# Optimization experiments

Measured on AMD Instinct MI355X. Metric: run time of the kernel, lower is better.

## Reference

```python
import jax, jax.numpy as jnp
import numpy as np

FIELD_DIMS = [26000] * 39
EMBED_DIM = 64
MLP_DIMS = [400, 400, 400]
BATCH = 16384
OFFSETS = jnp.asarray(np.concatenate(([0], np.cumsum(FIELD_DIMS)[:-1])), dtype=jnp.int32)
BN_INV = 1.0 / np.sqrt(1.0 + 1e-5)  # eval-mode BatchNorm1d: running_mean=0, running_var=1


def setup_inputs() -> dict:
    key = jax.random.key(0)
    ks = jax.random.split(key, 16)
    B, F, E = BATCH, len(FIELD_DIMS), EMBED_DIM
    V = sum(FIELD_DIMS)
    s = lambda k, shp, sc=0.05: (jax.random.normal(k, shp, jnp.float32) * sc)
    inp = {
        "x": jax.random.randint(ks[0], (B, F), 0, FIELD_DIMS[0], dtype=jnp.int32),
        "emb_table": s(ks[1], (V, E)),
        "lin_table": s(ks[2], (V, 1)),
        "lin_bias": jnp.zeros((1,), jnp.float32),
        "sparse_var": s(ks[3], (F, E), 0.1),
        "Wt": s(ks[4], (F, E, E)),  # per-field Linear weights, (out,in) layout
        "bt": jnp.zeros((F, E), jnp.float32),
    }
    dims = [F * E] + MLP_DIMS
    for i in range(3):
        inp[f"W{i+1}"] = s(ks[5 + i], (dims[i], dims[i + 1]))
        inp[f"b{i+1}"] = jnp.zeros((dims[i + 1],), jnp.float32)
        inp[f"g{i+1}"] = jnp.ones((dims[i + 1],), jnp.float32)
        inp[f"be{i+1}"] = jnp.zeros((dims[i + 1],), jnp.float32)
    inp["Wout"] = s(ks[9], (MLP_DIMS[-1], 1))
    inp["bout"] = jnp.zeros((1,), jnp.float32)
    return inp


def reference(x, emb_table, lin_table, lin_bias, sparse_var, Wt, bt,
              W1, b1, g1, be1, W2, b2, g2, be2, W3, b3, g3, be3, Wout, bout):
    B = x.shape[0]
    idx = x + OFFSETS[None, :]                       # (B, F) global vocab ids
    # sparse gate (detached in torch), eval-mode hard threshold mask
    sv = jax.nn.sigmoid(jax.lax.stop_gradient(sparse_var) * 15.0)
    sv = jnp.where(sv > 0.001, sv, 0.0)              # (F, E)
    embed_x = emb_table[idx] * sv                    # (B, F, E) gather + gate
    # per-field small Linear, batched as one einsum (torch: y = e @ W.T + b)
    trans = jnp.einsum('bfi,foi->bfo', embed_x, Wt) + bt  # (B, F, E)
    # FM second-order term
    sum_f = trans.sum(axis=1)                        # (B, E)
    fm = 0.5 * jnp.sum(sum_f * sum_f - (trans * trans).sum(axis=1),
                       axis=-1, keepdims=True)       # (B, 1)
    # first-order linear term
    lin = lin_table[idx].sum(axis=1) + lin_bias      # (B, 1)
    # MLP on flattened gated embeddings (Linear -> BN(eval) -> ReLU)
    h = embed_x.reshape(B, -1)
    for W, b, g, be in ((W1, b1, g1, be1), (W2, b2, g2, be2), (W3, b3, g3, be3)):
        h = jax.nn.relu((h @ W + b) * (BN_INV * g) + be)
    mlp = h @ Wout + bout                            # (B, 1)
    return jax.nn.sigmoid(jnp.squeeze(lin + fm + mlp, axis=1))  # (B,)
```

## Files before the change

kernel.cpp:

```cpp
#include <hip/hip_runtime.h>

#define BT 16384
#define NF 39
#define FD 26000

typedef unsigned short u16;
typedef unsigned int u32;
typedef short bf16x8 __attribute__((ext_vector_type(8)));
typedef float f32x4 __attribute__((ext_vector_type(4)));

__device__ __forceinline__ float bf2f(u16 h) {
  union { u32 u; float f; } v; v.u = ((u32)h) << 16; return v.f;
}
__device__ __forceinline__ u16 f2bf(float f) {
  union { float f; u32 u; } v; v.f = f;
  u32 r = v.u + 0x7fffu + ((v.u >> 16) & 1u);
  return (u16)(r >> 16);
}

__device__ __forceinline__ void gld16(const u16* g, u16* l) {
  __builtin_amdgcn_global_load_lds(
      (const __attribute__((address_space(1))) void*)g,
      (__attribute__((address_space(3))) void*)l, 16, 0, 0);
}

__global__ __launch_bounds__(256) void k_embed(
    const int* __restrict__ x, const float* __restrict__ emb,
    const float* __restrict__ lin_table, const float* __restrict__ lin_bias,
    const float* __restrict__ sparse_var, const float* __restrict__ Wt,
    const float* __restrict__ bt, u16* __restrict__ h0, float* __restrict__ base)
{
  __shared__ u16                s_x[32 * NF];
  __shared__ float              s_sv[NF * 64];
  __shared__ float              s_bt[NF * 64];
  __shared__ __align__(16) u16  s_emb[32 * 72];
  __shared__ __align__(16) u16  s_wt[64 * 72];
  __shared__ float              s_S[32 * 65];
  __shared__ float              s_Qp[64];
  __shared__ float              s_lin[32];

  const int tid = threadIdx.x;
  const int b0 = blockIdx.x * 32;

  for (int i = tid; i < 32 * NF; i += 256) s_x[i] = (u16)x[b0 * NF + i];
  for (int i = tid; i < NF * 64; i += 256) {
    float v = sparse_var[i];
    float s = 1.0f / (1.0f + __expf(-15.0f * v));
    s_sv[i] = (s > 0.001f) ? s : 0.0f;
    s_bt[i] = bt[i];
  }
  __syncthreads();

  const int wave = tid >> 6, lane = tid & 63;
  const int quad = lane >> 4, c16 = lane & 15;
  const int mt = wave & 1, nh = wave >> 1;

  float q[4] = {0.f, 0.f, 0.f, 0.f};
  float accS[2][4];
  #pragma unroll
  for (int j = 0; j < 2; ++j)
    #pragma unroll
    for (int r = 0; r < 4; ++r) accS[j][r] = 0.f;

  const int g_row = tid >> 3, g_c8 = (tid & 7) * 8;

  for (int f = 0; f < NF; ++f) {
    #pragma unroll
    for (int it = 0; it < 2; ++it) {
      int row = g_row + it * 32;
      float4 w0 = *(const float4*)&Wt[f * 4096 + row * 64 + g_c8];
      float4 w1 = *(const float4*)&Wt[f * 4096 + row * 64 + g_c8 + 4];
      union { uint4 v; u16 h[8]; } p;
      p.h[0] = f2bf(w0.x); p.h[1] = f2bf(w0.y); p.h[2] = f2bf(w0.z); p.h[3] = f2bf(w0.w);
      p.h[4] = f2bf(w1.x); p.h[5] = f2bf(w1.y); p.h[6] = f2bf(w1.z); p.h[7] = f2bf(w1.w);
      *(uint4*)&s_wt[row * 72 + g_c8] = p.v;
    }
    {
      long gi = (long)((int)s_x[g_row * NF + f] + f * FD);
      float4 e0 = *(const float4*)&emb[gi * 64 + g_c8];
      float4 e1 = *(const float4*)&emb[gi * 64 + g_c8 + 4];
      union { uint4 v; u16 h[8]; } p;
      p.h[0] = f2bf(e0.x * s_sv[f * 64 + g_c8 + 0]);
      p.h[1] = f2bf(e0.y * s_sv[f * 64 + g_c8 + 1]);
      p.h[2] = f2bf(e0.z * s_sv[f * 64 + g_c8 + 2]);
      p.h[3] = f2bf(e0.w * s_sv[f * 64 + g_c8 + 3]);
      p.h[4] = f2bf(e1.x * s_sv[f * 64 + g_c8 + 4]);
      p.h[5] = f2bf(e1.y * s_sv[f * 64 + g_c8 + 5]);
      p.h[6] = f2bf(e1.z * s_sv[f * 64 + g_c8 + 6]);
      p.h[7] = f2bf(e1.w * s_sv[f * 64 + g_c8 + 7]);
      *(uint4*)&s_emb[g_row * 72 + g_c8] = p.v;
      *(uint4*)&h0[(long)(b0 + g_row) * 2496 + f * 64 + g_c8] = p.v;
    }
    __syncthreads();

    bf16x8 a0 = *(const bf16x8*)&s_emb[(mt * 16 + c16) * 72 + quad * 8];
    bf16x8 a1 = *(const bf16x8*)&s_emb[(mt * 16 + c16) * 72 + 32 + quad * 8];
    #pragma unroll
    for (int j = 0; j < 2; ++j) {
      int nt = nh * 2 + j;
      bf16x8 bb0 = *(const bf16x8*)&s_wt[(nt * 16 + c16) * 72 + quad * 8];
      bf16x8 bb1 = *(const bf16x8*)&s_wt[(nt * 16 + c16) * 72 + 32 + quad * 8];
      f32x4 acc = {0.f, 0.f, 0.f, 0.f};
      acc = __builtin_amdgcn_mfma_f32_16x16x32_bf16(a0, bb0, acc, 0, 0, 0);
      acc = __builtin_amdgcn_mfma_f32_16x16x32_bf16(a1, bb1, acc, 0, 0, 0);
      float btv = s_bt[f * 64 + nt * 16 + c16];
      #pragma unroll
      for (int r = 0; r < 4; ++r) {
        float t = acc[r] + btv;
        accS[j][r] += t;
        q[r] += t * t;
      }
    }
    __syncthreads();
  }

  #pragma unroll
  for (int j = 0; j < 2; ++j)
    #pragma unroll
    for (int r = 0; r < 4; ++r)
      s_S[(mt * 16 + quad * 4 + r) * 65 + (nh * 2 + j) * 16 + c16] = accS[j][r];

  #pragma unroll
  for (int r = 0; r < 4; ++r) {
    float v = q[r];
    v += __shfl_xor(v, 1, 64);
    v += __shfl_xor(v, 2, 64);
    v += __shfl_xor(v, 4, 64);
    v += __shfl_xor(v, 8, 64);
    if (c16 == 0) s_Qp[nh * 32 + mt * 16 + quad * 4 + r] = v;
  }

  {
    int row = tid >> 3, fi = tid & 7;
    float lv = 0.f;
    for (int f = fi; f < NF; f += 8)
      lv += lin_table[(int)s_x[row * NF + f] + f * FD];
    lv += __shfl_xor(lv, 1, 64);
    lv += __shfl_xor(lv, 2, 64);
    lv += __shfl_xor(lv, 4, 64);
    if (fi == 0) s_lin[row] = lv;
  }
  __syncthreads();

  if (tid < 32) {
    float s2 = 0.f;
    #pragma unroll 8
    for (int e = 0; e < 64; ++e) { float v = s_S[tid * 65 + e]; s2 += v * v; }
    float fmv = 0.5f * (s2 - (s_Qp[tid] + s_Qp[32 + tid]));
    base[b0 + tid] = s_lin[tid] + lin_bias[0] + fmv;
  }
}

__global__ __launch_bounds__(256) void k_gemm(
    const u16* __restrict__ A, int lda, const u16* __restrict__ Bt, int ldb,
    int kit, const float* __restrict__ bias, const float* __restrict__ g,
    const float* __restrict__ be, u16* __restrict__ C, int ldc)
{
  __shared__ __align__(16) u16 sA[128 * 64];
  __shared__ __align__(16) u16 sB[80 * 64];

  const int tid = threadIdx.x;
  int bid = blockIdx.x;
  int xcd = bid & 7;
  int j = bid >> 3;
  const int m0 = (xcd * 16 + j / 5) * 128;
  const int n0 = (j % 5) * 80;

  const int wave = tid >> 6, lane = tid & 63;
  const int quad = lane >> 4, c16 = lane & 15;

  const int srow = lane >> 3;
  const int sclog = (lane & 7) ^ (srow & 7);
  const u16* gA = A + (long)m0 * lda + sclog * 8;
  const u16* gB = Bt + (long)n0 * ldb + sclog * 8;

  f32x4 acc[2][5];
  #pragma unroll
  for (int mtt = 0; mtt < 2; ++mtt)
    #pragma unroll
    for (int nt = 0; nt < 5; ++nt) acc[mtt][nt] = {0.f, 0.f, 0.f, 0.f};

  for (int kk = 0; kk < kit; ++kk) {
    const int k0 = kk * 64;
    #pragma unroll
    for (int it = 0; it < 4; ++it) {
      int s = wave * 4 + it;
      gld16(gA + (long)(s * 8 + srow) * lda + k0, &sA[s * 512]);
    }
    gld16(gB + (long)(wave * 8 + srow) * ldb + k0, &sB[wave * 512]);
    gld16(gB + (long)((wave + 4) * 8 + srow) * ldb + k0, &sB[(wave + 4) * 512]);
    if (wave < 2)
      gld16(gB + (long)((wave + 8) * 8 + srow) * ldb + k0, &sB[(wave + 8) * 512]);
    __syncthreads();

    #pragma unroll
    for (int ks = 0; ks < 2; ++ks) {
      const int co = ((ks * 4 + quad) ^ (c16 & 7)) * 8;
      bf16x8 a0 = *(const bf16x8*)&sA[(wave * 32 + c16) * 64 + co];
      bf16x8 a1 = *(const bf16x8*)&sA[(wave * 32 + 16 + c16) * 64 + co];
      #pragma unroll
      for (int nt = 0; nt < 5; ++nt) {
        bf16x8 b = *(const bf16x8*)&sB[(nt * 16 + c16) * 64 + co];
        acc[0][nt] = __builtin_amdgcn_mfma_f32_16x16x32_bf16(a0, b, acc[0][nt], 0, 0, 0);
        acc[1][nt] = __builtin_amdgcn_mfma_f32_16x16x32_bf16(a1, b, acc[1][nt], 0, 0, 0);
      }
    }
    __syncthreads();
  }

  const float BN_INV = 0.9999950000374997f;
  #pragma unroll
  for (int nt = 0; nt < 5; ++nt) {
    int col = n0 + nt * 16 + c16;
    float bb = bias[col];
    float sc = BN_INV * g[col];
    float bv = be[col];
    #pragma unroll
    for (int mtt = 0; mtt < 2; ++mtt) {
      #pragma unroll
      for (int r = 0; r < 4; ++r) {
        int row = m0 + wave * 32 + mtt * 16 + quad * 4 + r;
        float y = (acc[mtt][nt][r] + bb) * sc + bv;
        y = fmaxf(y, 0.f);
        C[(long)row * ldc + col] = f2bf(y);
      }
    }
  }
  if (ldc > 400 && n0 == 320) {
    int npad = ldc - 400;
    for (int s = tid; s < 128 * npad; s += 256) {
      int rr = s / npad, cc = s % npad;
      C[(long)(m0 + rr) * ldc + 400 + cc] = 0;
    }
  }
}

__global__ __launch_bounds__(256) void k_transpose3(
    const float* __restrict__ W1, u16* __restrict__ W1T,
    const float* __restrict__ W2, u16* __restrict__ W2T,
    const float* __restrict__ W3, u16* __restrict__ W3T)
{
  int z = blockIdx.z;
  const float* in = (z == 0) ? W1 : (z == 1) ? W2 : W3;
  u16* out = (z == 0) ? W1T : (z == 1) ? W2T : W3T;
  int R = (z == 0) ? 2496 : 400;
  int Rpad = (z == 0) ? 2496 : 448;
  const int C = 400;
  int r0 = blockIdx.y * 32, c0 = blockIdx.x * 32;
  if (r0 >= Rpad) return;
  __shared__ u16 t[32][33];
  int tx = threadIdx.x & 31, ty = threadIdx.x >> 5;
  for (int i = ty; i < 32; i += 8) {
    int r = r0 + i, c = c0 + tx;
    t[i][tx] = (r < R && c < C) ? f2bf(in[(long)r * C + c]) : (u16)0;
  }
  __syncthreads();
  for (int i = ty; i < 32; i += 8) {
    int c = c0 + i, r = r0 + tx;
    if (c < C && r < Rpad) out[(long)c * Rpad + r] = t[tx][i];
  }
}

__global__ __launch_bounds__(256) void k_final(
    const u16* __restrict__ h3, const float* __restrict__ Wout,
    const float* __restrict__ bout, const float* __restrict__ base,
    float* __restrict__ out)
{
  int wave = threadIdx.x >> 6, lane = threadIdx.x & 63;
  int b = blockIdx.x * 4 + wave;
  float s = 0.f;
  for (int jj = lane; jj < 400; jj += 64)
    s += bf2f(h3[(long)b * 448 + jj]) * Wout[jj];
  #pragma unroll
  for (int m = 32; m >= 1; m >>= 1) s += __shfl_xor(s, m, 64);
  if (lane == 0) {
    float z = s + base[b] + bout[0];
    out[b] = 1.0f / (1.0f + __expf(-z));
  }
}

extern "C" void kernel_launch(void* const* d_in, const int* in_sizes, int n_in,
                              void* d_out, int out_size, void* d_ws, size_t ws_size,
                              hipStream_t stream)
{
  const int*   x         = (const int*)d_in[0];
  const float* emb       = (const float*)d_in[1];
  const float* lin_table = (const float*)d_in[2];
  const float* lin_bias  = (const float*)d_in[3];
  const float* svar      = (const float*)d_in[4];
  const float* Wt        = (const float*)d_in[5];
  const float* bt        = (const float*)d_in[6];
  const float* W1  = (const float*)d_in[7];
  const float* b1  = (const float*)d_in[8];
  const float* g1  = (const float*)d_in[9];
  const float* be1 = (const float*)d_in[10];
  const float* W2  = (const float*)d_in[11];
  const float* b2  = (const float*)d_in[12];
  const float* g2  = (const float*)d_in[13];
  const float* be2 = (const float*)d_in[14];
  const float* W3  = (const float*)d_in[15];
  const float* b3  = (const float*)d_in[16];
  const float* g3  = (const float*)d_in[17];
  const float* be3 = (const float*)d_in[18];
  const float* Wo  = (const float*)d_in[19];
  const float* bo  = (const float*)d_in[20];

  char* ws = (char*)d_ws;
  size_t off = 0;
  u16* h0 = (u16*)(ws + off);   off += (size_t)BT * 2496 * 2;
  u16* h1 = (u16*)(ws + off);   off += (size_t)BT * 448 * 2;
  u16* h2 = (u16*)(ws + off);   off += (size_t)BT * 448 * 2;
  u16* h3 = (u16*)(ws + off);   off += (size_t)BT * 448 * 2;
  float* base = (float*)(ws + off); off += (size_t)BT * 4;
  u16* W1T = (u16*)(ws + off);  off += (size_t)400 * 2496 * 2;
  u16* W2T = (u16*)(ws + off);  off += (size_t)400 * 448 * 2;
  u16* W3T = (u16*)(ws + off);  off += (size_t)400 * 448 * 2;
  (void)ws_size; (void)in_sizes; (void)n_in; (void)out_size;

  k_transpose3<<<dim3(13, 78, 3), 256, 0, stream>>>(W1, W1T, W2, W2T, W3, W3T);
  k_embed<<<512, 256, 0, stream>>>(x, emb, lin_table, lin_bias, svar, Wt, bt,
                                   h0, base);
  k_gemm<<<640, 256, 0, stream>>>(h0, 2496, W1T, 2496, 39, b1, g1, be1, h1, 448);
  k_gemm<<<640, 256, 0, stream>>>(h1, 448, W2T, 448, 7, b2, g2, be2, h2, 448);
  k_gemm<<<640, 256, 0, stream>>>(h2, 448, W3T, 448, 7, b3, g3, be3, h3, 448);
  k_final<<<4096, 256, 0, stream>>>(h3, Wo, bo, base, (float*)d_out);
}
```

Baseline: 480.0 us.

## Fuse embedding with first MLP layer and fuse remaining layers into one tail kernel

The embedding/FM kernel now also computes the first MLP GEMM directly from the gated embeddings held in shared memory, so the large h0 activation is no longer written to or read from global memory. Layers two and three plus the output dot product and sigmoid are merged into a single per-32-row kernel that keeps activations in swizzled LDS. The per-field Wt matrices are converted to bf16 once in a prep kernel, and the weight transposes are padded to 448 columns. The trade-off is that each block handles only 32 rows, so W1 (about 2 MB) is re-streamed by all 512 blocks. Each wave also holds 14 accumulator tiles, which raises register pressure and may reduce occupancy.

```diff
diff --git a/kernel.cpp b/kernel.cpp
--- a/kernel.cpp
+++ b/kernel.cpp
@@ -17,26 +17,75 @@
   u32 r = v.u + 0x7fffu + ((v.u >> 16) & 1u);
   return (u16)(r >> 16);
 }
-
 __device__ __forceinline__ void gld16(const u16* g, u16* l) {
   __builtin_amdgcn_global_load_lds(
       (const __attribute__((address_space(1))) void*)g,
       (__attribute__((address_space(3))) void*)l, 16, 0, 0);
 }
-
-__global__ __launch_bounds__(256) void k_embed(
+__device__ __forceinline__ int swz4(int n) { return (n ^ (n >> 2)) & 3; }
+
+__device__ __forceinline__ void stage_w448(const u16* WT, long ld, int k0,
+                                           u16* s_w, int wave, int lane) {
+  int rlo = lane >> 2, clo = lane & 3;
+  #pragma unroll
+  for (int i = wave; i < 28; i += 4) {
+    int n = i * 16 + rlo;
+    int c = clo ^ swz4(n);
+    gld16(WT + (long)n * ld + k0 + c * 8, &s_w[i * 512]);
+  }
+}
+__device__ __forceinline__ bf16x8 read_b448(const u16* s_w, int n, int quad) {
+  int c = quad ^ swz4(n);
+  return *(const bf16x8*)&s_w[n * 32 + c * 8];
+}
+
+__global__ __launch_bounds__(256) void k_prep(
+    const float* __restrict__ W1, u16* __restrict__ W1T,
+    const float* __restrict__ W2, u16* __restrict__ W2T,
+    const float* __restrict__ W3, u16* __restrict__ W3T,
+    const float* __restrict__ Wt, u16* __restrict__ Wtb)
+{
+  int z = blockIdx.z;
+  if (z == 3) {
+    int idx = (blockIdx.y * 14 + blockIdx.x) * 256 + threadIdx.x;
+    if (idx < NF * 4096) Wtb[idx] = f2bf(Wt[idx]);
+    return;
+  }
+  const float* in = (z == 0) ? W1 : (z == 1) ? W2 : W3;
+  u16* outp = (z == 0) ? W1T : (z == 1) ? W2T : W3T;
+  int K = (z == 0) ? 2496 : 400;
+  int Kpad = (z == 0) ? 2496 : 448;
+  int r0 = blockIdx.y * 32, c0 = blockIdx.x * 32;
+  if (r0 >= Kpad) return;
+  __shared__ u16 t[32][33];
+  int tx = threadIdx.x & 31, ty = threadIdx.x >> 5;
+  for (int i = ty; i < 32; i += 8) {
+    int r = r0 + i, c = c0 + tx;
+    t[i][tx] = (r < K && c < 400) ? f2bf(in[(long)r * 400 + c]) : (u16)0;
+  }
+  __syncthreads();
+  int r = r0 + tx;
+  if (r < Kpad)
+    for (int i = ty; i < 32; i += 8)
+      outp[(long)(c0 + i) * Kpad + r] = t[tx][i];
+}
+
+__global__ __launch_bounds__(256) void k_fused1(
     const int* __restrict__ x, const float* __restrict__ emb,
     const float* __restrict__ lin_table, const float* __restrict__ lin_bias,
-    const float* __restrict__ sparse_var, const float* __restrict__ Wt,
-    const float* __restrict__ bt, u16* __restrict__ h0, float* __restrict__ base)
+    const float* __restrict__ sparse_var, const u16* __restrict__ Wtb,
+    const float* __restrict__ bt, const u16* __restrict__ W1T,
+    const float* __restrict__ b1, const float* __restrict__ g1,
+    const float* __restrict__ be1, u16* __restrict__ h1,
+    float* __restrict__ base)
 {
   __shared__ u16                s_x[32 * NF];
   __shared__ float              s_sv[NF * 64];
   __shared__ float              s_bt[NF * 64];
   __shared__ __align__(16) u16  s_emb[32 * 72];
-  __shared__ __align__(16) u16  s_wt[64 * 72];
-  __shared__ float              s_S[32 * 65];
-  __shared__ float              s_Qp[64];
+  __shared__ __align__(16) u16  s_wt[64 * 64];
+  __shared__ __align__(16) u16  s_w[448 * 32];
+  __shared__ float              s_fm[64];
   __shared__ float              s_lin[32];
 
   const int tid = threadIdx.x;
@@ -54,26 +103,20 @@
   const int wave = tid >> 6, lane = tid & 63;
   const int quad = lane >> 4, c16 = lane & 15;
   const int mt = wave & 1, nh = wave >> 1;
-
+  const int g_row = tid >> 3, g_c8 = (tid & 7) * 8;
+
+  f32x4 acc1[14];
+  #pragma unroll
+  for (int nt = 0; nt < 14; ++nt) acc1[nt] = {0.f, 0.f, 0.f, 0.f};
   float q[4] = {0.f, 0.f, 0.f, 0.f};
-  float accS[2][4];
-  #pragma unroll
-  for (int j = 0; j < 2; ++j)
-    #pragma unroll
-    for (int r = 0; r < 4; ++r) accS[j][r] = 0.f;
-
-  const int g_row = tid >> 3, g_c8 = (tid & 7) * 8;
+  float accS[2][4] = {{0.f,0.f,0.f,0.f},{0.f,0.f,0.f,0.f}};
 
   for (int f = 0; f < NF; ++f) {
-    #pragma unroll
-    for (int it = 0; it < 2; ++it) {
-      int row = g_row + it * 32;
-      float4 w0 = *(const float4*)&Wt[f * 4096 + row * 64 + g_c8];
-      float4 w1 = *(const float4*)&Wt[f * 4096 + row * 64 + g_c8 + 4];
-      union { uint4 v; u16 h[8]; } p;
-      p.h[0] = f2bf(w0.x); p.h[1] = f2bf(w0.y); p.h[2] = f2bf(w0.z); p.h[3] = f2bf(w0.w);
-      p.h[4] = f2bf(w1.x); p.h[5] = f2bf(w1.y); p.h[6] = f2bf(w1.z); p.h[7] = f2bf(w1.w);
-      *(uint4*)&s_wt[row * 72 + g_c8] = p.v;
+    stage_w448(W1T, 2496, f * 64, s_w, wave, lane);
+    #pragma unroll
+    for (int i = 0; i < 2; ++i) {
+      int ii = wave * 2 + i;
+      gld16(Wtb + f * 4096 + ii * 512 + lane * 8, &s_wt[ii * 512]);
     }
     {
       long gi = (long)((int)s_x[g_row * NF + f] + f * FD);
@@ -89,17 +132,17 @@
       p.h[6] = f2bf(e1.z * s_sv[f * 64 + g_c8 + 6]);
       p.h[7] = f2bf(e1.w * s_sv[f * 64 + g_c8 + 7]);
       *(uint4*)&s_emb[g_row * 72 + g_c8] = p.v;
-      *(uint4*)&h0[(long)(b0 + g_row) * 2496 + f * 64 + g_c8] = p.v;
     }
     __syncthreads();
 
     bf16x8 a0 = *(const bf16x8*)&s_emb[(mt * 16 + c16) * 72 + quad * 8];
     bf16x8 a1 = *(const bf16x8*)&s_emb[(mt * 16 + c16) * 72 + 32 + quad * 8];
+
     #pragma unroll
     for (int j = 0; j < 2; ++j) {
       int nt = nh * 2 + j;
-      bf16x8 bb0 = *(const bf16x8*)&s_wt[(nt * 16 + c16) * 72 + quad * 8];
-      bf16x8 bb1 = *(const bf16x8*)&s_wt[(nt * 16 + c16) * 72 + 32 + quad * 8];
+      bf16x8 bb0 = *(const bf16x8*)&s_wt[(nt * 16 + c16) * 64 + quad * 8];
+      bf16x8 bb1 = *(const bf16x8*)&s_wt[(nt * 16 + c16) * 64 + 32 + quad * 8];
       f32x4 acc = {0.f, 0.f, 0.f, 0.f};
       acc = __builtin_amdgcn_mfma_f32_16x16x32_bf16(a0, bb0, acc, 0, 0, 0);
       acc = __builtin_amdgcn_mfma_f32_16x16x32_bf16(a1, bb1, acc, 0, 0, 0);
@@ -111,25 +154,33 @@
         q[r] += t * t;
       }
     }
+    #pragma unroll
+    for (int nt = 0; nt < 14; ++nt) {
+      int n = nh * 224 + nt * 16 + c16;
+      acc1[nt] = __builtin_amdgcn_mfma_f32_16x16x32_bf16(
+          a0, read_b448(s_w, n, quad), acc1[nt], 0, 0, 0);
+    }
     __syncthreads();
-  }
-
-  #pragma unroll
-  for (int j = 0; j < 2; ++j)
-    #pragma unroll
-    for (int r = 0; r < 4; ++r)
-      s_S[(mt * 16 + quad * 4 + r) * 65 + (nh * 2 + j) * 16 + c16] = accS[j][r];
+    stage_w448(W1T, 2496, f * 64 + 32, s_w, wave, lane);
+    __syncthreads();
+    #pragma unroll
+    for (int nt = 0; nt < 14; ++nt) {
+      int n = nh * 224 + nt * 16 + c16;
+      acc1[nt] = __builtin_amdgcn_mfma_f32_16x16x32_bf16(
+          a1, read_b448(s_w, n, quad), acc1[nt], 0, 0, 0);
+    }
+    __syncthreads();
+  }
 
   #pragma unroll
   for (int r = 0; r < 4; ++r) {
-    float v = q[r];
+    float v = accS[0][r] * accS[0][r] + accS[1][r] * accS[1][r] - q[r];
     v += __shfl_xor(v, 1, 64);
     v += __shfl_xor(v, 2, 64);
     v += __shfl_xor(v, 4, 64);
     v += __shfl_xor(v, 8, 64);
-    if (c16 == 0) s_Qp[nh * 32 + mt * 16 + quad * 4 + r] = v;
-  }
-
+    if (c16 == 0) s_fm[nh * 32 + mt * 16 + quad * 4 + r] = v;
+  }
   {
     int row = tid >> 3, fi = tid & 7;
     float lv = 0.f;
@@ -141,141 +192,130 @@
     if (fi == 0) s_lin[row] = lv;
   }
   __syncthreads();
-
-  if (tid < 32) {
-    float s2 = 0.f;
-    #pragma unroll 8
-    for (int e = 0; e < 64; ++e) { float v = s_S[tid * 65 + e]; s2 += v * v; }
-    float fmv = 0.5f * (s2 - (s_Qp[tid] + s_Qp[32 + tid]));
-    base[b0 + tid] = s_lin[tid] + lin_bias[0] + fmv;
-  }
-}
-
-__global__ __launch_bounds__(256) void k_gemm(
-    const u16* __restrict__ A, int lda, const u16* __restrict__ Bt, int ldb,
-    int kit, const float* __restrict__ bias, const float* __restrict__ g,
-    const float* __restrict__ be, u16* __restrict__ C, int ldc)
+  if (tid < 32)
+    base[b0 + tid] = s_lin[tid] + lin_bias[0]
+                   + 0.5f * (s_fm[tid] + s_fm[32 + tid]);
+
+  const float BN_INV = 0.9999950000374997f;
+  #pragma unroll
+  for (int nt = 0; nt < 14; ++nt) {
+    int col = nh * 224 + nt * 16 + c16;
+    bool valid = col < 400;
+    float bb = valid ? b1[col] : 0.f;
+    float sc = valid ? BN_INV * g1[col] : 0.f;
+    float bv = valid ? be1[col] : 0.f;
+    #pragma unroll
+    for (int r = 0; r < 4; ++r) {
+      int row = b0 + mt * 16 + quad * 4 + r;
+      float y = valid ? fmaxf((acc1[nt][r] + bb) * sc + bv, 0.f) : 0.f;
+      h1[(long)row * 448 + col] = f2bf(y);
+    }
+  }
+}
+
+__global__ __launch_bounds__(256) void k_tail(
+    const u16* __restrict__ h1, const u16* __restrict__ W2T,
+    const u16* __restrict__ W3T,
+    const float* __restrict__ b2, const float* __restrict__ g2,
+    const float* __restrict__ be2,
+    const float* __restrict__ b3, const float* __restrict__ g3,
+    const float* __restrict__ be3,
+    const float* __restrict__ Wout, const float* __restrict__ bout,
+    const float* __restrict__ base, float* __restrict__ out)
 {
-  __shared__ __align__(16) u16 sA[128 * 64];
-  __shared__ __align__(16) u16 sB[80 * 64];
+  __shared__ __align__(16) u16 s_h[32 * 448];
+  __shared__ __align__(16) u16 s_w[448 * 32];
+  __shared__ float s_wout[448];
+  __shared__ float s_red[64];
 
   const int tid = threadIdx.x;
-  int bid = blockIdx.x;
-  int xcd = bid & 7;
-  int j = bid >> 3;
-  const int m0 = (xcd * 16 + j / 5) * 128;
-  const int n0 = (j % 5) * 80;
+  const int b0 = blockIdx.x * 32;
+  for (int i = tid; i < 448; i += 256) s_wout[i] = (i < 400) ? Wout[i] : 0.f;
+  for (int s = tid; s < 1792; s += 256) {
+    int flat = s * 8;
+    int row = flat / 448;
+    int kc = (flat - row * 448) >> 3;
+    int pc = (kc & 0x38) | ((kc ^ row) & 7);
+    uint4 v = *(const uint4*)&h1[(long)b0 * 448 + flat];
+    *(uint4*)&s_h[row * 448 + pc * 8] = v;
+  }
+  __syncthreads();
 
   const int wave = tid >> 6, lane = tid & 63;
   const int quad = lane >> 4, c16 = lane & 15;
-
-  const int srow = lane >> 3;
-  const int sclog = (lane & 7) ^ (srow & 7);
-  const u16* gA = A + (long)m0 * lda + sclog * 8;
-  const u16* gB = Bt + (long)n0 * ldb + sclog * 8;
-
-  f32x4 acc[2][5];
-  #pragma unroll
-  for (int mtt = 0; mtt < 2; ++mtt)
-    #pragma unroll
-    for (int nt = 0; nt < 5; ++nt) acc[mtt][nt] = {0.f, 0.f, 0.f, 0.f};
-
-  for (int kk = 0; kk < kit; ++kk) {
-    const int k0 = kk * 64;
-    #pragma unroll
-    for (int it = 0; it < 4; ++it) {
-      int s = wave * 4 + it;
-      gld16(gA + (long)(s * 8 + srow) * lda + k0, &sA[s * 512]);
-    }
-    gld16(gB + (long)(wave * 8 + srow) * ldb + k0, &sB[wave * 512]);
-    gld16(gB + (long)((wave + 4) * 8 + srow) * ldb + k0, &sB[(wave + 4) * 512]);
-    if (wave < 2)
-      gld16(gB + (long)((wave + 8) * 8 + srow) * ldb + k0, &sB[(wave + 8) * 512]);
-    __syncthreads();
-
-    #pragma unroll
-    for (int ks = 0; ks < 2; ++ks) {
-      const int co = ((ks * 4 + quad) ^ (c16 & 7)) * 8;
-      bf16x8 a0 = *(const bf16x8*)&sA[(wave * 32 + c16) * 64 + co];
-      bf16x8 a1 = *(const bf16x8*)&sA[(wave * 32 + 16 + c16) * 64 + co];
+  const int mt = wave & 1, nh = wave >> 1;
+  const int m = mt * 16 + c16;
+  const float BN_INV = 0.9999950000374997f;
+
+  f32x4 acc[14];
+  float p[4] = {0.f, 0.f, 0.f, 0.f};
+
+  for (int layer = 0; layer < 2; ++layer) {
+    const u16* WT = layer ? W3T : W2T;
+    #pragma unroll
+    for (int nt = 0; nt < 14; ++nt) acc[nt] = {0.f, 0.f, 0.f, 0.f};
+    for (int ks = 0; ks < 14; ++ks) {
+      stage_w448(WT, 448, ks * 32, s_w, wave, lane);
+      __syncthreads();
+      int kc = ks * 4 + quad;
+      int pc = (kc & 0x38) | ((kc ^ m) & 7);
+      bf16x8 a = *(const bf16x8*)&s_h[m * 448 + pc * 8];
       #pragma unroll
-      for (int nt = 0; nt < 5; ++nt) {
-        bf16x8 b = *(const bf16x8*)&sB[(nt * 16 + c16) * 64 + co];
-        acc[0][nt] = __builtin_amdgcn_mfma_f32_16x16x32_bf16(a0, b, acc[0][nt], 0, 0, 0);
-        acc[1][nt] = __builtin_amdgcn_mfma_f32_16x16x32_bf16(a1, b, acc[1][nt], 0, 0, 0);
+      for (int nt = 0; nt < 14; ++nt) {
+        int n = nh * 224 + nt * 16 + c16;
+        acc[nt] = __builtin_amdgcn_mfma_f32_16x16x32_bf16(
+            a, read_b448(s_w, n, quad), acc[nt], 0, 0, 0);
       }
-    }
-    __syncthreads();
-  }
-
-  const float BN_INV = 0.9999950000374997f;
-  #pragma unroll
-  for (int nt = 0; nt < 5; ++nt) {
-    int col = n0 + nt * 16 + c16;
-    float bb = bias[col];
-    float sc = BN_INV * g[col];
-    float bv = be[col];
-    #pragma unroll
-    for (int mtt = 0; mtt < 2; ++mtt) {
+      __syncthreads();
+    }
+    if (layer == 0) {
       #pragma unroll
-      for (int r = 0; r < 4; ++r) {
-        int row = m0 + wave * 32 + mtt * 16 + quad * 4 + r;
-        float y = (acc[mtt][nt][r] + bb) * sc + bv;
-        y = fmaxf(y, 0.f);
-        C[(long)row * ldc + col] = f2bf(y);
+      for (int nt = 0; nt < 14; ++nt) {
+        int col = nh * 224 + nt * 16 + c16;
+        bool valid = col < 400;
+        float bb = valid ? b2[col] : 0.f;
+        float sc = valid ? BN_INV * g2[col] : 0.f;
+        float bv = valid ? be2[col] : 0.f;
+        int kc = col >> 3;
+        #pragma unroll
+        for (int r = 0; r < 4; ++r) {
+          int row = mt * 16 + quad * 4 + r;
+          float y = valid ? fmaxf((acc[nt][r] + bb) * sc + bv, 0.f) : 0.f;
+          int pc = (kc & 0x38) | ((kc ^ row) & 7);
+          s_h[row * 448 + pc * 8 + (col & 7)] = f2bf(y);
+        }
       }
-    }
-  }
-  if (ldc > 400 && n0 == 320) {
-    int npad = ldc - 400;
-    for (int s = tid; s < 128 * npad; s += 256) {
-      int rr = s / npad, cc = s % npad;
-      C[(long)(m0 + rr) * ldc + 400 + cc] = 0;
-    }
-  }
-}
-
-__global__ __launch_bounds__(256) void k_transpose3(
-    const float* __restrict__ W1, u16* __restrict__ W1T,
-    const float* __restrict__ W2, u16* __restrict__ W2T,
-    const float* __restrict__ W3, u16* __restrict__ W3T)
-{
-  int z = blockIdx.z;
-  const float* in = (z == 0) ? W1 : (z == 1) ? W2 : W3;
-  u16* out = (z == 0) ? W1T : (z == 1) ? W2T : W3T;
-  int R = (z == 0) ? 2496 : 400;
-  int Rpad = (z == 0) ? 2496 : 448;
-  const int C = 400;
-  int r0 = blockIdx.y * 32, c0 = blockIdx.x * 32;
-  if (r0 >= Rpad) return;
-  __shared__ u16 t[32][33];
-  int tx = threadIdx.x & 31, ty = threadIdx.x >> 5;
-  for (int i = ty; i < 32; i += 8) {
-    int r = r0 + i, c = c0 + tx;
-    t[i][tx] = (r < R && c < C) ? f2bf(in[(long)r * C + c]) : (u16)0;
-  }
-  __syncthreads();
-  for (int i = ty; i < 32; i += 8) {
-    int c = c0 + i, r = r0 + tx;
-    if (c < C && r < Rpad) out[(long)c * Rpad + r] = t[tx][i];
-  }
-}
-
-__global__ __launch_bounds__(256) void k_final(
-    const u16* __restrict__ h3, const float* __restrict__ Wout,
-    const float* __restrict__ bout, const float* __restrict__ base,
-    float* __restrict__ out)
-{
-  int wave = threadIdx.x >> 6, lane = threadIdx.x & 63;
-  int b = blockIdx.x * 4 + wave;
-  float s = 0.f;
-  for (int jj = lane; jj < 400; jj += 64)
-    s += bf2f(h3[(long)b * 448 + jj]) * Wout[jj];
-  #pragma unroll
-  for (int m = 32; m >= 1; m >>= 1) s += __shfl_xor(s, m, 64);
-  if (lane == 0) {
-    float z = s + base[b] + bout[0];
-    out[b] = 1.0f / (1.0f + __expf(-z));
+      __syncthreads();
+    } else {
+      #pragma unroll
+      for (int nt = 0; nt < 14; ++nt) {
+        int col = nh * 224 + nt * 16 + c16;
+        bool valid = col < 400;
+        float bb = valid ? b3[col] : 0.f;
+        float sc = valid ? BN_INV * g3[col] : 0.f;
+        float bv = valid ? be3[col] : 0.f;
+        float w = s_wout[col];
+        #pragma unroll
+        for (int r = 0; r < 4; ++r) {
+          float y = valid ? fmaxf((acc[nt][r] + bb) * sc + bv, 0.f) : 0.f;
+          p[r] += y * w;
+        }
+      }
+    }
+  }
+  #pragma unroll
+  for (int r = 0; r < 4; ++r) {
+    float v = p[r];
+    v += __shfl_xor(v, 1, 64);
+    v += __shfl_xor(v, 2, 64);
+    v += __shfl_xor(v, 4, 64);
+    v += __shfl_xor(v, 8, 64);
+    if (c16 == 0) s_red[nh * 32 + mt * 16 + quad * 4 + r] = v;
+  }
+  __syncthreads();
+  if (tid < 32) {
+    float z = base[b0 + tid] + s_red[tid] + s_red[32 + tid] + bout[0];
+    out[b0 + tid] = 1.0f / (1.0f + __expf(-z));
   }
 }
 
@@ -307,21 +347,17 @@
 
   char* ws = (char*)d_ws;
   size_t off = 0;
-  u16* h0 = (u16*)(ws + off);   off += (size_t)BT * 2496 * 2;
-  u16* h1 = (u16*)(ws + off);   off += (size_t)BT * 448 * 2;
-  u16* h2 = (u16*)(ws + off);   off += (size_t)BT * 448 * 2;
-  u16* h3 = (u16*)(ws + off);   off += (size_t)BT * 448 * 2;
+  u16* h1 = (u16*)(ws + off);     off += (size_t)BT * 448 * 2;
   float* base = (float*)(ws + off); off += (size_t)BT * 4;
-  u16* W1T = (u16*)(ws + off);  off += (size_t)400 * 2496 * 2;
-  u16* W2T = (u16*)(ws + off);  off += (size_t)400 * 448 * 2;
-  u16* W3T = (u16*)(ws + off);  off += (size_t)400 * 448 * 2;
+  u16* W1T = (u16*)(ws + off);    off += (size_t)448 * 2496 * 2;
+  u16* W2T = (u16*)(ws + off);    off += (size_t)448 * 448 * 2;
+  u16* W3T = (u16*)(ws + off);    off += (size_t)448 * 448 * 2;
+  u16* Wtb = (u16*)(ws + off);    off += (size_t)NF * 4096 * 2;
   (void)ws_size; (void)in_sizes; (void)n_in; (void)out_size;
 
-  k_transpose3<<<dim3(13, 78, 3), 256, 0, stream>>>(W1, W1T, W2, W2T, W3, W3T);
-  k_embed<<<512, 256, 0, stream>>>(x, emb, lin_table, lin_bias, svar, Wt, bt,
-                                   h0, base);
-  k_gemm<<<640, 256, 0, stream>>>(h0, 2496, W1T, 2496, 39, b1, g1, be1, h1, 448);
-  k_gemm<<<640, 256, 0, stream>>>(h1, 448, W2T, 448, 7, b2, g2, be2, h2, 448);
-  k_gemm<<<640, 256, 0, stream>>>(h2, 448, W3T, 448, 7, b3, g3, be3, h3, 448);
-  k_final<<<4096, 256, 0, stream>>>(h3, Wo, bo, base, (float*)d_out);
-}
+  k_prep<<<dim3(14, 78, 4), 256, 0, stream>>>(W1, W1T, W2, W2T, W3, W3T, Wt, Wtb);
+  k_fused1<<<512, 256, 0, stream>>>(x, emb, lin_table, lin_bias, svar, Wtb, bt,
+                                    W1T, b1, g1, be1, h1, base);
+  k_tail<<<512, 256, 0, stream>>>(h1, W2T, W3T, b2, g2, be2, b3, g3, be3,
+                                  Wo, bo, base, (float*)d_out);
+}
```

New measurement: 520.1 us. 8.4% more time.
